# Kernel tuning notes

Measured on AMD Instinct MI355X. Metric: run time of the kernel, lower is better.

The kernel has to match this reference:

```python
import jax, jax.numpy as jnp
import numpy as np

N_NODES, N_EDGES, N_REL, F_DIM, N_HEAD, N_LAYERS = 20000, 100000, 1000, 128, 4, 4
NEG_SLOPE = 0.2  # PyG GATv2Conv default negative_slope


def _gatv2_layer(x, ea_full, src, dst, Wl, bl, Wr, br, We, att, bias):
    # x: [N, F]; ea_full: [Etot, F] edge attrs (incl. self-loop rows)
    N = x.shape[0]
    H, C = att.shape  # heads, out-dim per head
    xl = (x @ Wl + bl).reshape(N, H, C)          # source-side projection
    xr = (x @ Wr + br).reshape(N, H, C)          # target-side projection
    ee = (ea_full @ We).reshape(-1, H, C)        # [Etot, H, C] edge embedding
    # GATv2 scoring: leaky_relu(x_i + x_j + e) . att
    e = jax.nn.leaky_relu(xl[src] + xr[dst] + ee, NEG_SLOPE)
    logits = jnp.einsum('ehc,hc->eh', e, att)    # [Etot, H]
    # segment softmax over edges grouped by destination node
    m = jax.ops.segment_max(logits, dst, num_segments=N)
    p = jnp.exp(logits - m[dst])
    denom = jax.ops.segment_sum(p, dst, num_segments=N)
    alpha = p / denom[dst]                       # [Etot, H]
    out = jax.ops.segment_sum(alpha[:, :, None] * xl[src], dst, num_segments=N)
    return out.mean(axis=1) + bias               # concat=False -> head mean


def setup_inputs() -> dict:
    key = jax.random.key(0)
    ks = jax.random.split(key, 12)
    N, E, R, F, H, L = N_NODES, N_EDGES, N_REL, F_DIM, N_HEAD, N_LAYERS
    HC = H * F
    s = 1.0 / np.sqrt(F)
    return {
        'x': jax.random.normal(ks[0], (N, F), jnp.float32),
        'edge_index': jax.random.randint(ks[1], (2, E), 0, N, dtype=jnp.int32),
        'relations': jax.random.normal(ks[2], (R, F), jnp.float32),
        'relation_index': jax.random.randint(ks[3], (E,), 0, R, dtype=jnp.int32),
        'Wl': jax.random.normal(ks[4], (L, F, HC), jnp.float32) * s,
        'bl': jnp.zeros((L, HC), jnp.float32),
        'Wr': jax.random.normal(ks[5], (L, F, HC), jnp.float32) * s,
        'br': jnp.zeros((L, HC), jnp.float32),
        'We': jax.random.normal(ks[6], (L, F, HC), jnp.float32) * s,
        'att': jax.random.normal(ks[7], (L, H, F), jnp.float32) * s,
        'bias': jnp.zeros((L, F), jnp.float32),
    }


def reference(x, edge_index, relations, relation_index, Wl, bl, Wr, br, We, att, bias):
    N = x.shape[0]
    sl = jnp.arange(N, dtype=edge_index.dtype)
    src = jnp.concatenate([edge_index[0], sl])   # add_self_loops=True
    dst = jnp.concatenate([edge_index[1], sl])
    ea = relations[relation_index]               # [E, F]
    # self-loop edge_attr uses fill_value='mean' (PyG default)
    ea_mean = ea.mean(axis=0)
    ea_full = jnp.concatenate([ea, jnp.broadcast_to(ea_mean, (N, ea.shape[1]))])
    h = x
    for l in range(N_LAYERS):
        h = _gatv2_layer(h, ea_full, src, dst, Wl[l], bl[l], Wr[l], br[l], We[l], att[l], bias[l])
    return (h, relations)
```

## Files before the change

kernel.cpp:

```cpp
#include <hip/hip_runtime.h>
#include <hip/hip_bf16.h>

#define N_NODES   20000
#define N_EDGES   100000
#define N_REL     1000
#define F_DIM     128
#define N_HEAD    4
#define HC        512
#define HC2       256
#define N_LAYERS  4
#define REL_EXT_ROWS 1008
#define NEG_SLOPE 0.2f

typedef __attribute__((ext_vector_type(8))) short short8;
typedef __attribute__((ext_vector_type(4))) float floatx4;

__device__ __forceinline__ float loadIn(const void* p, size_t i, int f32) {
    if (f32) return ((const float*)p)[i];
    union { unsigned int u; float f; } c;
    c.u = ((unsigned int)((const unsigned short*)p)[i]) << 16;
    return c.f;
}

__device__ __forceinline__ unsigned short f2bf(float v) {
    __hip_bfloat16 b = __float2bfloat16(v);
    return *(unsigned short*)&b;
}

__device__ __forceinline__ void unpack2(unsigned int u, float& lo, float& hi) {
    union { unsigned int u; float f; } a, b;
    a.u = u << 16;
    b.u = u & 0xFFFF0000u;
    lo = a.f; hi = b.f;
}

__global__ void detect_kernel(const unsigned short* __restrict__ x, int* __restrict__ flag) {
    int t = threadIdx.x;
    int cnt = 0;
    for (int j = t; j < 256; j += 64) {
        int e = (x[j] >> 7) & 0xFF;
        if (e >= 143) cnt++;
    }
    for (int off = 32; off; off >>= 1) cnt += __shfl_xor(cnt, off);
    if (t == 0) flag[0] = (cnt >= 8) ? 1 : 0;
}


__global__ void hist_kernel(const int* __restrict__ dst, const int* __restrict__ rel,
                            int* __restrict__ deg, int* __restrict__ rcount) {
    int e = blockIdx.x * 256 + threadIdx.x;
    if (e < N_EDGES) {
        atomicAdd(&deg[dst[e]], 1);
        atomicAdd(&rcount[rel[e]], 1);
    }
}

__global__ void ea_mean_kernel(const int* __restrict__ rcount,
                               const void* __restrict__ relations,
                               float* __restrict__ ea_mean, const int* __restrict__ flag) {
    int f32 = flag[0];
    int b = blockIdx.x;
    int t = threadIdx.x;
    int col = t & 127;
    int rhalf = t >> 7;
    float acc = 0.f;
    for (int j = 0; j < 4; ++j) {
        int r = b * 8 + j * 2 + rhalf;
        acc += (float)rcount[r] * loadIn(relations, (size_t)r * F_DIM + col, f32);
    }
    __shared__ float part[256];
    part[t] = acc;
    __syncthreads();
    if (t < 128)
        atomicAdd(&ea_mean[col], (part[t] + part[t + 128]) * (1.f / (float)N_EDGES));
}

__global__ void relext_kernel(const void* __restrict__ relations,
                              const float* __restrict__ ea_mean,
                              unsigned short* __restrict__ rel_ext, const int* __restrict__ flag) {
    int idx = blockIdx.x * 256 + threadIdx.x;
    if (idx >= REL_EXT_ROWS * F_DIM) return;
    int f32 = flag[0];
    int r = idx >> 7;
    int c = idx & 127;
    float v;
    if (r < N_REL)       v = loadIn(relations, idx, f32);
    else if (r == N_REL) v = ea_mean[c];
    else                 v = 0.f;
    rel_ext[idx] = f2bf(v);
}

__global__ void scan_kernel(const int* __restrict__ deg,
                            int* __restrict__ row_start, int* __restrict__ cursor) {
    __shared__ int part[1024];
    int t = threadIdx.x;
    const int CH = (N_NODES + 1023) / 1024;
    int base = t * CH;
    int sum = 0;
    for (int j = 0; j < CH; ++j) {
        int idx = base + j;
        if (idx < N_NODES) sum += deg[idx];
    }
    part[t] = sum;
    __syncthreads();
    for (int off = 1; off < 1024; off <<= 1) {
        int u = (t >= off) ? part[t - off] : 0;
        __syncthreads();
        part[t] += u;
        __syncthreads();
    }
    int run = part[t] - sum;
    for (int j = 0; j < CH; ++j) {
        int idx = base + j;
        if (idx < N_NODES) {
            row_start[idx] = run;
            cursor[idx] = run;
            run += deg[idx];
        }
    }
    if (t == 1023) row_start[N_NODES] = part[1023];
}

__global__ void scatter_kernel(const int* __restrict__ src, const int* __restrict__ dst,
                               const int* __restrict__ rel, int* __restrict__ cursor,
                               int* __restrict__ csr_pack) {
    int e = blockIdx.x * 256 + threadIdx.x;
    if (e < N_EDGES) {
        int d = dst[e];
        int p = atomicAdd(&cursor[d], 1);
        csr_pack[p] = src[e] | (rel[e] << 16);
    }
}

__global__ void tail_kernel(const void* __restrict__ relations, void* __restrict__ out,
                            const int* __restrict__ flag) {
    int i = blockIdx.x * 256 + threadIdx.x;
    if (i >= N_REL * F_DIM) return;
    int f32 = flag[0];
    float v = loadIn(relations, i, f32);
    size_t o = (size_t)N_NODES * F_DIM + i;
    if (f32) ((float*)out)[o] = v;
    else     ((unsigned short*)out)[o] = f2bf(v);
}

__global__ void w_transpose_kernel(const void* __restrict__ Wl, const void* __restrict__ Wr,
                                   const void* __restrict__ We,
                                   unsigned short* __restrict__ Wt, const int* __restrict__ flag) {
    int f32 = flag[0];
    int k0 = blockIdx.x * 64;
    int n0 = blockIdx.y * 64;
    int mat = blockIdx.z;
    const void* src = (mat < 4) ? Wl : (mat < 8 ? Wr : We);
    size_t base = (size_t)(mat & 3) * F_DIM * HC;
    unsigned short* dst = Wt + (size_t)mat * HC * F_DIM;
    __shared__ float T[64][65];
    int t = threadIdx.x;
    int r = t >> 2, cq = t & 3;
    for (int j = 0; j < 16; ++j) {
        int n = cq * 16 + j;
        T[n][r] = loadIn(src, base + (size_t)(k0 + r) * HC + n0 + n, f32);
    }
    __syncthreads();
    for (int j = 0; j < 16; ++j) {
        int k = cq * 16 + j;
        dst[(size_t)(n0 + r) * F_DIM + k0 + k] = f2bf(T[r][k]);
    }
}

__launch_bounds__(256, 4)
__global__ void proj_kernel(const void* __restrict__ A, int a_input, int M,
                            const unsigned short* __restrict__ Wt0,
                            const unsigned short* __restrict__ Wt1,
                            const void* __restrict__ bias0, size_t b0_off,
                            const void* __restrict__ bias1, size_t b1_off,
                            unsigned short* __restrict__ out0,
                            unsigned short* __restrict__ out1,
                            int tpb, const int* __restrict__ flag) {
    __shared__ __align__(16) short As[64][136];
    __shared__ __align__(16) short BtRaw[128 * 72];
    int f32 = flag[0];
    int a_f32 = a_input ? f32 : 0;
    int m0 = blockIdx.x * 64;
    int t = threadIdx.x;

    for (int j = 0; j < 4; ++j) {
        int c = t + j * 256;
        int row = c >> 4;
        int colc = (c & 15) * 8;
        int gm = m0 + row;
        short8 v = (short8){0, 0, 0, 0, 0, 0, 0, 0};
        if (gm < M) {
            size_t idx = (size_t)gm * F_DIM + colc;
            if (a_f32) {
                const float* Af = (const float*)A;
                for (int q = 0; q < 8; ++q) v[q] = (short)f2bf(Af[idx + q]);
            } else {
                v = *(const short8*)((const unsigned short*)A + idx);
            }
        }
        *(short8*)&As[row][colc] = v;
    }

    int wave = t >> 6, lane = t & 63;
    int wm = (wave >> 1) * 32, wn = (wave & 1) * 64;
    int r16 = lane & 15, quad = lane >> 4;

    for (int it = 0; it < tpb; ++it) {
        int nt = blockIdx.y * tpb + it;
        const unsigned short* Wt = (nt < 4) ? Wt0 : Wt1;
        int n0 = (nt & 3) * 128;

        floatx4 acc[2][4];
        for (int mi = 0; mi < 2; ++mi)
            for (int ni = 0; ni < 4; ++ni)
                acc[mi][ni] = (floatx4){0.f, 0.f, 0.f, 0.f};

        for (int half = 0; half < 2; ++half) {
            __syncthreads();
            for (int j = 0; j < 4; ++j) {
                int c = t + j * 256;
                int nl = c >> 3;
                int kc = (c & 7) * 8;
                *(short8*)&BtRaw[nl * 72 + kc] =
                    *(const short8*)(Wt + (size_t)(n0 + nl) * F_DIM + half * 64 + kc);
            }
            __syncthreads();

            for (int kk = 0; kk < 2; ++kk) {
                short8 a[2], b[4];
                for (int mi = 0; mi < 2; ++mi)
                    a[mi] = *(const short8*)&As[wm + mi * 16 + r16][half * 64 + kk * 32 + quad * 8];
                for (int ni = 0; ni < 4; ++ni)
                    b[ni] = *(const short8*)&BtRaw[(wn + ni * 16 + r16) * 72 + kk * 32 + quad * 8];
                for (int mi = 0; mi < 2; ++mi)
                    for (int ni = 0; ni < 4; ++ni)
                        acc[mi][ni] = __builtin_amdgcn_mfma_f32_16x16x32_bf16(a[mi], b[ni], acc[mi][ni], 0, 0, 0);
            }
        }

        const void* bias = (nt < 4) ? bias0 : bias1;
        size_t boff = (nt < 4) ? b0_off : b1_off;
        unsigned short* out = (nt < 4) ? out0 : out1;
        __syncthreads();
        for (int mi = 0; mi < 2; ++mi) {
            for (int ni = 0; ni < 4; ++ni) {
                int col = wn + ni * 16 + r16;
                float bv = bias ? loadIn(bias, boff + n0 + col, f32) : 0.f;
                for (int r = 0; r < 4; ++r) {
                    int rowl = wm + mi * 16 + quad * 4 + r;
                    BtRaw[rowl * 136 + col] = (short)f2bf(acc[mi][ni][r] + bv);
                }
            }
        }
        __syncthreads();
        for (int j = 0; j < 4; ++j) {
            int c = t + j * 256;
            int rowl = c >> 4;
            int colc = (c & 15) * 8;
            int gm = m0 + rowl;
            if (gm < M)
                *(short8*)(out + (size_t)gm * HC + n0 + colc) =
                    *(const short8*)&BtRaw[rowl * 136 + colc];
        }
    }
}

__launch_bounds__(256)
__global__ void edge_kernel(const unsigned int* __restrict__ xl2,
                            const unsigned int* __restrict__ xr2,
                            const unsigned int* __restrict__ re2,
                            const int* __restrict__ row_start,
                            const int* __restrict__ csr_pack,
                            const void* __restrict__ att, size_t att_off,
                            const void* __restrict__ bias, size_t bias_off,
                            void* __restrict__ hout, int final_layer,
                            const int* __restrict__ flag) {
    int f32 = flag[0];
    int i = blockIdx.x;
    int h = threadIdx.x >> 6;
    int lane = threadIdx.x & 63;
    int pidx = h * 64 + lane;

    float xr0, xr1; unpack2(xr2[(size_t)i * HC2 + pidx], xr0, xr1);
    float a0 = loadIn(att, att_off + h * F_DIM + 2 * lane, f32);
    float a1 = loadIn(att, att_off + h * F_DIM + 2 * lane + 1, f32);
    float er0, er1; unpack2(re2[(size_t)N_REL * HC2 + pidx], er0, er1);

    float xs0, xs1; unpack2(xl2[(size_t)i * HC2 + pidx], xs0, xs1);
    float t0 = xs0 + xr0 + er0;
    float t1 = xs1 + xr1 + er1;
    t0 = (t0 > 0.f) ? t0 : NEG_SLOPE * t0;
    t1 = (t1 > 0.f) ? t1 : NEG_SLOPE * t1;
    float m = t0 * a0 + t1 * a1;
    for (int off = 32; off; off >>= 1) m += __shfl_xor(m, off);
    float s = 1.f, acc0 = xs0, acc1 = xs1;

    int e0 = row_start[i], e1 = row_start[i + 1];
    if (e0 < 0) e0 = 0;
    if (e1 > N_EDGES) e1 = N_EDGES;
    if (e1 < e0) e1 = e0;

    unsigned int xlv = 0, rev = 0;
    if (e0 < e1) {
        int pk = csr_pack[e0];
        int src = pk & 0xFFFF;  if (src >= N_NODES) src = 0;
        int rr  = (pk >> 16) & 0x3FF; if (rr > N_REL) rr = N_REL;
        xlv = xl2[(size_t)src * HC2 + pidx];
        rev = re2[(size_t)rr * HC2 + pidx];
    }
    for (int e = e0; e < e1; ++e) {
        unsigned int xlvn = 0, revn = 0;
        if (e + 1 < e1) {
            int pkn = csr_pack[e + 1];
            int sn = pkn & 0xFFFF;  if (sn >= N_NODES) sn = 0;
            int rn = (pkn >> 16) & 0x3FF; if (rn > N_REL) rn = N_REL;
            xlvn = xl2[(size_t)sn * HC2 + pidx];
            revn = re2[(size_t)rn * HC2 + pidx];
        }
        float xl0, xl1; unpack2(xlv, xl0, xl1);
        float ee0, ee1; unpack2(rev, ee0, ee1);
        float u0 = xl0 + xr0 + ee0;
        float u1 = xl1 + xr1 + ee1;
        u0 = (u0 > 0.f) ? u0 : NEG_SLOPE * u0;
        u1 = (u1 > 0.f) ? u1 : NEG_SLOPE * u1;
        float part = u0 * a0 + u1 * a1;
        for (int off = 32; off; off >>= 1) part += __shfl_xor(part, off);
        float mn = fmaxf(m, part);
        float sc = __expf(m - mn);
        float p  = __expf(part - mn);
        s = s * sc + p;
        acc0 = acc0 * sc + p * xl0;
        acc1 = acc1 * sc + p * xl1;
        m = mn;
        xlv = xlvn; rev = revn;
    }

    float inv = 1.f / s;
    __shared__ float lsum[N_HEAD][F_DIM];
    lsum[h][2 * lane]     = acc0 * inv;
    lsum[h][2 * lane + 1] = acc1 * inv;
    __syncthreads();
    if (threadIdx.x < F_DIM) {
        int c = threadIdx.x;
        float v = (lsum[0][c] + lsum[1][c] + lsum[2][c] + lsum[3][c]) * 0.25f
                + loadIn(bias, bias_off + c, f32);
        size_t o = (size_t)i * F_DIM + c;
        if (final_layer && f32) ((float*)hout)[o] = v;
        else                    ((unsigned short*)hout)[o] = f2bf(v);
    }
}


extern "C" void kernel_launch(void* const* d_in, const int* in_sizes, int n_in,
                              void* d_out, int out_size, void* d_ws, size_t ws_size,
                              hipStream_t stream) {
    const void* x          = d_in[0];
    const int*  edge_index = (const int*)d_in[1];
    const void* relations  = d_in[2];
    const int*  rel_index  = (const int*)d_in[3];
    const void* Wl         = d_in[4];
    const void* bl         = d_in[5];
    const void* Wr         = d_in[6];
    const void* br         = d_in[7];
    const void* We         = d_in[8];
    const void* att        = d_in[9];
    const void* bias       = d_in[10];

    char* ws = (char*)d_ws;
    size_t off = 0;
    auto alloc = [&](size_t bytes) -> void* {
        void* p = ws + off;
        off = (off + bytes + 255) & ~(size_t)255;
        return p;
    };
    int*            flag     = (int*)alloc(4);
    int*            deg      = (int*)alloc(N_NODES * 4);
    int*            row_start= (int*)alloc((N_NODES + 1) * 4);
    int*            cursor   = (int*)alloc(N_NODES * 4);
    int*            rcount   = (int*)alloc(N_REL * 4);
    float*          ea_mean  = (float*)alloc(F_DIM * 4);
    int*            csr_pack = (int*)alloc(N_EDGES * 4);
    unsigned short* rel_ext  = (unsigned short*)alloc((size_t)REL_EXT_ROWS * F_DIM * 2);
    unsigned short* Wt       = (unsigned short*)alloc((size_t)12 * HC * F_DIM * 2);
    unsigned short* re       = (unsigned short*)alloc((size_t)REL_EXT_ROWS * HC * 2);
    unsigned short* hbuf     = (unsigned short*)alloc((size_t)N_NODES * F_DIM * 2);
    unsigned short* xl       = (unsigned short*)alloc((size_t)N_NODES * HC * 2);
    unsigned short* xr       = (unsigned short*)alloc((size_t)N_NODES * HC * 2);

    const int* esrc = edge_index;
    const int* edst = edge_index + N_EDGES;

    detect_kernel<<<1, 64, 0, stream>>>((const unsigned short*)x, flag);
    hipMemsetAsync(rcount, 0, N_REL * 4, stream);
    hipMemsetAsync(deg, 0, N_NODES * 4, stream);
    hipMemsetAsync(ea_mean, 0, F_DIM * 4, stream);
    hist_kernel<<<(N_EDGES + 255) / 256, 256, 0, stream>>>(edst, rel_index, deg, rcount);
    ea_mean_kernel<<<N_REL / 8, 256, 0, stream>>>(rcount, relations, ea_mean, flag);
    relext_kernel<<<(REL_EXT_ROWS * F_DIM + 255) / 256, 256, 0, stream>>>(relations, ea_mean, rel_ext, flag);
    scan_kernel<<<1, 1024, 0, stream>>>(deg, row_start, cursor);
    scatter_kernel<<<(N_EDGES + 255) / 256, 256, 0, stream>>>(esrc, edst, rel_index, cursor, csr_pack);
    w_transpose_kernel<<<dim3(2, 8, 12), 256, 0, stream>>>(Wl, Wr, We, Wt, flag);
    tail_kernel<<<(N_REL * F_DIM + 255) / 256, 256, 0, stream>>>(relations, d_out, flag);

    const void* hin = x;
    int a_input = 1;
    for (int l = 0; l < N_LAYERS; ++l) {
        const unsigned short* Wlt = Wt + (size_t)l * HC * F_DIM;
        const unsigned short* Wrt = Wt + (size_t)(4 + l) * HC * F_DIM;
        const unsigned short* Wet = Wt + (size_t)(8 + l) * HC * F_DIM;
        proj_kernel<<<dim3((N_NODES + 63) / 64, 4), 256, 0, stream>>>(
            hin, a_input, N_NODES, Wlt, Wrt,
            bl, (size_t)l * HC, br, (size_t)l * HC,
            xl, xr, 2, flag);
        proj_kernel<<<dim3((REL_EXT_ROWS + 63) / 64, 4), 256, 0, stream>>>(
            rel_ext, 0, REL_EXT_ROWS, Wet, nullptr,
            nullptr, 0, nullptr, 0,
            re, nullptr, 1, flag);
        int final_layer = (l == N_LAYERS - 1);
        void* hout = final_layer ? d_out : (void*)hbuf;
        edge_kernel<<<N_NODES, 256, 0, stream>>>((const unsigned int*)xl, (const unsigned int*)xr,
                                                 (const unsigned int*)re, row_start, csr_pack,
                                                 att, (size_t)l * N_HEAD * F_DIM,
                                                 bias, (size_t)l * F_DIM,
                                                 hout, final_layer, flag);
        hin = hbuf;
        a_input = 0;
    }
}
```

Measured before the change: 494.7 us.

## Parallelize edge softmax across wavefronts with chunked two-pass shared-memory logits

The edge kernel now spreads a node's incoming edges across the four wavefronts. Each wavefront handles a whole edge row using 16-byte vector loads, so all four heads are covered in one load, instead of one wavefront per head walking every edge serially. Logits are staged in shared memory in chunks of up to 256 edges, and a block-wide max/sum pass produces the softmax weights. A second pass re-gathers the source features to accumulate the weighted sums, and the partial sums are then reduced across wavefronts. This removes the serial, latency-bound online-softmax loop but adds extra gathers of xl, more block synchronisations and more shared-memory traffic.

Result: slower. 701.3 us (+41.8%).

```diff
diff --git a/kernel.cpp b/kernel.cpp
--- a/kernel.cpp
+++ b/kernel.cpp
@@ -11,6 +11,7 @@
 #define N_LAYERS  4
 #define REL_EXT_ROWS 1008
 #define NEG_SLOPE 0.2f
+#define MAXE      256
 
 typedef __attribute__((ext_vector_type(8))) short short8;
 typedef __attribute__((ext_vector_type(4))) float floatx4;
@@ -275,75 +276,130 @@
                             const void* __restrict__ bias, size_t bias_off,
                             void* __restrict__ hout, int final_layer,
                             const int* __restrict__ flag) {
+    __shared__ float l_log[N_HEAD][MAXE];
+    __shared__ float l_acc[N_HEAD][HC / N_HEAD * N_HEAD];
+    __shared__ float s_run[N_HEAD], m_run[N_HEAD], chunk_sc[N_HEAD];
+
     int f32 = flag[0];
     int i = blockIdx.x;
-    int h = threadIdx.x >> 6;
-    int lane = threadIdx.x & 63;
-    int pidx = h * 64 + lane;
-
-    float xr0, xr1; unpack2(xr2[(size_t)i * HC2 + pidx], xr0, xr1);
-    float a0 = loadIn(att, att_off + h * F_DIM + 2 * lane, f32);
-    float a1 = loadIn(att, att_off + h * F_DIM + 2 * lane + 1, f32);
-    float er0, er1; unpack2(re2[(size_t)N_REL * HC2 + pidx], er0, er1);
-
-    float xs0, xs1; unpack2(xl2[(size_t)i * HC2 + pidx], xs0, xs1);
-    float t0 = xs0 + xr0 + er0;
-    float t1 = xs1 + xr1 + er1;
-    t0 = (t0 > 0.f) ? t0 : NEG_SLOPE * t0;
-    t1 = (t1 > 0.f) ? t1 : NEG_SLOPE * t1;
-    float m = t0 * a0 + t1 * a1;
-    for (int off = 32; off; off >>= 1) m += __shfl_xor(m, off);
-    float s = 1.f, acc0 = xs0, acc1 = xs1;
+    int t = threadIdx.x;
+    int w = t >> 6, lane = t & 63;
+    int hl = lane >> 4;
+
+    const uint4* xl4 = (const uint4*)xl2;
+    const uint4* re4 = (const uint4*)re2;
+    const uint4* xr4 = (const uint4*)xr2;
+
+    float xrv[8], attv[8];
+    {
+        uint4 u = xr4[(size_t)i * 64 + lane];
+        unpack2(u.x, xrv[0], xrv[1]); unpack2(u.y, xrv[2], xrv[3]);
+        unpack2(u.z, xrv[4], xrv[5]); unpack2(u.w, xrv[6], xrv[7]);
+        for (int q = 0; q < 8; ++q)
+            attv[q] = loadIn(att, att_off + lane * 8 + q, f32);
+    }
+
+    if (t < N_HEAD) { s_run[t] = 0.f; m_run[t] = -3.0e38f; }
 
     int e0 = row_start[i], e1 = row_start[i + 1];
     if (e0 < 0) e0 = 0;
     if (e1 > N_EDGES) e1 = N_EDGES;
     if (e1 < e0) e1 = e0;
-
-    unsigned int xlv = 0, rev = 0;
-    if (e0 < e1) {
-        int pk = csr_pack[e0];
-        int src = pk & 0xFFFF;  if (src >= N_NODES) src = 0;
-        int rr  = (pk >> 16) & 0x3FF; if (rr > N_REL) rr = N_REL;
-        xlv = xl2[(size_t)src * HC2 + pidx];
-        rev = re2[(size_t)rr * HC2 + pidx];
-    }
-    for (int e = e0; e < e1; ++e) {
-        unsigned int xlvn = 0, revn = 0;
-        if (e + 1 < e1) {
-            int pkn = csr_pack[e + 1];
-            int sn = pkn & 0xFFFF;  if (sn >= N_NODES) sn = 0;
-            int rn = (pkn >> 16) & 0x3FF; if (rn > N_REL) rn = N_REL;
-            xlvn = xl2[(size_t)sn * HC2 + pidx];
-            revn = re2[(size_t)rn * HC2 + pidx];
-        }
-        float xl0, xl1; unpack2(xlv, xl0, xl1);
-        float ee0, ee1; unpack2(rev, ee0, ee1);
-        float u0 = xl0 + xr0 + ee0;
-        float u1 = xl1 + xr1 + ee1;
-        u0 = (u0 > 0.f) ? u0 : NEG_SLOPE * u0;
-        u1 = (u1 > 0.f) ? u1 : NEG_SLOPE * u1;
-        float part = u0 * a0 + u1 * a1;
-        for (int off = 32; off; off >>= 1) part += __shfl_xor(part, off);
-        float mn = fmaxf(m, part);
-        float sc = __expf(m - mn);
-        float p  = __expf(part - mn);
-        s = s * sc + p;
-        acc0 = acc0 * sc + p * xl0;
-        acc1 = acc1 * sc + p * xl1;
-        m = mn;
-        xlv = xlvn; rev = revn;
-    }
-
-    float inv = 1.f / s;
-    __shared__ float lsum[N_HEAD][F_DIM];
-    lsum[h][2 * lane]     = acc0 * inv;
-    lsum[h][2 * lane + 1] = acc1 * inv;
+    int total = (e1 - e0) + 1;
+    int nchunks = (total + MAXE - 1) / MAXE;
+
+    float acc[8];
+    for (int q = 0; q < 8; ++q) acc[q] = 0.f;
+
+    for (int ck = 0; ck < nchunks; ++ck) {
+        int start = ck * MAXE;
+        int cnt = total - start; if (cnt > MAXE) cnt = MAXE;
+        __syncthreads();
+
+        for (int slot = w; slot < cnt; slot += 4) {
+            int gs = start + slot;
+            int src, rr;
+            if (gs == 0) { src = i; rr = N_REL; }
+            else {
+                int pk = csr_pack[e0 + gs - 1];
+                src = pk & 0xFFFF;            if (src >= N_NODES) src = 0;
+                rr  = (pk >> 16) & 0x3FF;     if (rr > N_REL) rr = N_REL;
+            }
+            uint4 xu = xl4[(size_t)src * 64 + lane];
+            uint4 ru = re4[(size_t)rr * 64 + lane];
+            float xv[8], rv[8];
+            unpack2(xu.x, xv[0], xv[1]); unpack2(xu.y, xv[2], xv[3]);
+            unpack2(xu.z, xv[4], xv[5]); unpack2(xu.w, xv[6], xv[7]);
+            unpack2(ru.x, rv[0], rv[1]); unpack2(ru.y, rv[2], rv[3]);
+            unpack2(ru.z, rv[4], rv[5]); unpack2(ru.w, rv[6], rv[7]);
+            float part = 0.f;
+            for (int q = 0; q < 8; ++q) {
+                float u = xv[q] + xrv[q] + rv[q];
+                u = (u > 0.f) ? u : NEG_SLOPE * u;
+                part += u * attv[q];
+            }
+            for (int off = 8; off; off >>= 1) part += __shfl_xor(part, off);
+            if ((lane & 15) == 0) l_log[hl][slot] = part;
+        }
+        __syncthreads();
+
+        {
+            float cmax = -3.0e38f;
+            for (int sl = lane; sl < cnt; sl += 64) cmax = fmaxf(cmax, l_log[w][sl]);
+            for (int off = 32; off; off >>= 1) cmax = fmaxf(cmax, __shfl_xor(cmax, off));
+            float csum = 0.f;
+            for (int sl = lane; sl < cnt; sl += 64) {
+                float p = __expf(l_log[w][sl] - cmax);
+                l_log[w][sl] = p;
+                csum += p;
+            }
+            for (int off = 32; off; off >>= 1) csum += __shfl_xor(csum, off);
+            float mo = m_run[w];
+            float mn = fmaxf(mo, cmax);
+            float sc = __expf(mo - mn);
+            float fc = __expf(cmax - mn);
+            if (lane == 0) {
+                s_run[w] = s_run[w] * sc + fc * csum;
+                m_run[w] = mn;
+                chunk_sc[w] = sc;
+            }
+            for (int sl = lane; sl < cnt; sl += 64) l_log[w][sl] *= fc;
+        }
+        __syncthreads();
+
+        {
+            float scw = chunk_sc[hl];
+            for (int q = 0; q < 8; ++q) acc[q] *= scw;
+        }
+        for (int slot = w; slot < cnt; slot += 4) {
+            int gs = start + slot;
+            int src;
+            if (gs == 0) src = i;
+            else {
+                int pk = csr_pack[e0 + gs - 1];
+                src = pk & 0xFFFF; if (src >= N_NODES) src = 0;
+            }
+            uint4 xu = xl4[(size_t)src * 64 + lane];
+            float p = l_log[hl][slot];
+            float xv[8];
+            unpack2(xu.x, xv[0], xv[1]); unpack2(xu.y, xv[2], xv[3]);
+            unpack2(xu.z, xv[4], xv[5]); unpack2(xu.w, xv[6], xv[7]);
+            for (int q = 0; q < 8; ++q) acc[q] += p * xv[q];
+        }
+    }
+
     __syncthreads();
-    if (threadIdx.x < F_DIM) {
-        int c = threadIdx.x;
-        float v = (lsum[0][c] + lsum[1][c] + lsum[2][c] + lsum[3][c]) * 0.25f
-                + loadIn(bias, bias_off + c, f32);
+    for (int q = 0; q < 8; ++q) l_acc[w][lane * 8 + q] = acc[q];
+    __syncthreads();
+    if (t < F_DIM) {
+        int c = t;
+        float v = 0.f;
+        for (int h = 0; h < N_HEAD; ++h) {
+            float a = l_acc[0][h * F_DIM + c] + l_acc[1][h * F_DIM + c]
+                    + l_acc[2][h * F_DIM + c] + l_acc[3][h * F_DIM + c];
+            v += a / s_run[h];
+        }
+        v = v * 0.25f + loadIn(bias, bias_off + c, f32);
         size_t o = (size_t)i * F_DIM + c;
         if (final_layer && f32) ((float*)hout)[o] = v;
         else                    ((unsigned short*)hout)[o] = f2bf(v);
```

## Split fused edge kernel into edge-parallel scoring and node-parallel aggregation

Applied to the files above, without the earlier changes.

Replaces the per-node online-softmax edge kernel with two kernels. The first computes attention logits for every edge, including self-loops, with one wavefront per edge using 16-byte vector loads, and writes them to a logits buffer. The second does a two-pass softmax per destination node over the stored logits, then a weighted sum of gathered source features. This aims to parallelise scoring across edges instead of serialising it per node, at the cost of an extra launch per layer, a logits round trip through memory, a csr_dst array, and a second gather of xl in aggregation.

Result: slower. 923.1 us (+86.6%).

```diff
diff --git a/kernel.cpp b/kernel.cpp
--- a/kernel.cpp
+++ b/kernel.cpp
@@ -123,12 +123,13 @@
 
 __global__ void scatter_kernel(const int* __restrict__ src, const int* __restrict__ dst,
                                const int* __restrict__ rel, int* __restrict__ cursor,
-                               int* __restrict__ csr_pack) {
+                               int* __restrict__ csr_pack, int* __restrict__ csr_dst) {
     int e = blockIdx.x * 256 + threadIdx.x;
     if (e < N_EDGES) {
         int d = dst[e];
         int p = atomicAdd(&cursor[d], 1);
         csr_pack[p] = src[e] | (rel[e] << 16);
+        csr_dst[p] = d;
     }
 }
 
@@ -266,82 +267,103 @@
 }
 
 __launch_bounds__(256)
-__global__ void edge_kernel(const unsigned int* __restrict__ xl2,
-                            const unsigned int* __restrict__ xr2,
-                            const unsigned int* __restrict__ re2,
-                            const int* __restrict__ row_start,
-                            const int* __restrict__ csr_pack,
-                            const void* __restrict__ att, size_t att_off,
-                            const void* __restrict__ bias, size_t bias_off,
-                            void* __restrict__ hout, int final_layer,
-                            const int* __restrict__ flag) {
+__global__ void score_kernel(const uint4* __restrict__ xl4, const uint4* __restrict__ xr4,
+                             const uint4* __restrict__ re4,
+                             const int* __restrict__ csr_pack, const int* __restrict__ csr_dst,
+                             const void* __restrict__ att, size_t att_off,
+                             float* __restrict__ logits, const int* __restrict__ flag) {
+    int f32 = flag[0];
+    int w = threadIdx.x >> 6, lane = threadIdx.x & 63;
+    int v = blockIdx.x * 4 + w;
+    if (v >= N_EDGES + N_NODES) return;
+    int src, dst, rr;
+    if (v < N_EDGES) {
+        int pk = csr_pack[v];
+        src = pk & 0xFFFF;        if (src >= N_NODES) src = 0;
+        rr  = (pk >> 16) & 0x3FF; if (rr > N_REL) rr = N_REL;
+        dst = csr_dst[v];         if (dst < 0 || dst >= N_NODES) dst = 0;
+    } else {
+        src = dst = v - N_EDGES;
+        rr = N_REL;
+    }
+    uint4 xu = xl4[(size_t)src * 64 + lane];
+    uint4 yu = xr4[(size_t)dst * 64 + lane];
+    uint4 ru = re4[(size_t)rr * 64 + lane];
+    float xv[8], yv[8], rv[8];
+    unpack2(xu.x, xv[0], xv[1]); unpack2(xu.y, xv[2], xv[3]);
+    unpack2(xu.z, xv[4], xv[5]); unpack2(xu.w, xv[6], xv[7]);
+    unpack2(yu.x, yv[0], yv[1]); unpack2(yu.y, yv[2], yv[3]);
+    unpack2(yu.z, yv[4], yv[5]); unpack2(yu.w, yv[6], yv[7]);
+    unpack2(ru.x, rv[0], rv[1]); unpack2(ru.y, rv[2], rv[3]);
+    unpack2(ru.z, rv[4], rv[5]); unpack2(ru.w, rv[6], rv[7]);
+    float part = 0.f;
+    for (int q = 0; q < 8; ++q) {
+        float u = xv[q] + yv[q] + rv[q];
+        u = (u > 0.f) ? u : NEG_SLOPE * u;
+        part += u * loadIn(att, att_off + lane * 8 + q, f32);
+    }
+    for (int off = 8; off; off >>= 1) part += __shfl_xor(part, off);
+    if ((lane & 15) == 0) logits[(size_t)v * 4 + (lane >> 4)] = part;
+}
+
+__launch_bounds__(256)
+__global__ void agg_kernel(const unsigned int* __restrict__ xl2,
+                           const int* __restrict__ row_start,
+                           const int* __restrict__ csr_pack,
+                           const float* __restrict__ logits,
+                           const void* __restrict__ bias, size_t bias_off,
+                           void* __restrict__ hout, int final_layer,
+                           const int* __restrict__ flag) {
+    __shared__ float lsum[N_HEAD][F_DIM];
     int f32 = flag[0];
     int i = blockIdx.x;
-    int h = threadIdx.x >> 6;
-    int lane = threadIdx.x & 63;
-    int pidx = h * 64 + lane;
-
-    float xr0, xr1; unpack2(xr2[(size_t)i * HC2 + pidx], xr0, xr1);
-    float a0 = loadIn(att, att_off + h * F_DIM + 2 * lane, f32);
-    float a1 = loadIn(att, att_off + h * F_DIM + 2 * lane + 1, f32);
-    float er0, er1; unpack2(re2[(size_t)N_REL * HC2 + pidx], er0, er1);
-
-    float xs0, xs1; unpack2(xl2[(size_t)i * HC2 + pidx], xs0, xs1);
-    float t0 = xs0 + xr0 + er0;
-    float t1 = xs1 + xr1 + er1;
-    t0 = (t0 > 0.f) ? t0 : NEG_SLOPE * t0;
-    t1 = (t1 > 0.f) ? t1 : NEG_SLOPE * t1;
-    float m = t0 * a0 + t1 * a1;
-    for (int off = 32; off; off >>= 1) m += __shfl_xor(m, off);
-    float s = 1.f, acc0 = xs0, acc1 = xs1;
+    int t = threadIdx.x, w = t >> 6, lane = t & 63;
+    int pidx = w * 64 + lane;
 
     int e0 = row_start[i], e1 = row_start[i + 1];
     if (e0 < 0) e0 = 0;
     if (e1 > N_EDGES) e1 = N_EDGES;
     if (e1 < e0) e1 = e0;
-
-    unsigned int xlv = 0, rev = 0;
-    if (e0 < e1) {
-        int pk = csr_pack[e0];
-        int src = pk & 0xFFFF;  if (src >= N_NODES) src = 0;
-        int rr  = (pk >> 16) & 0x3FF; if (rr > N_REL) rr = N_REL;
-        xlv = xl2[(size_t)src * HC2 + pidx];
-        rev = re2[(size_t)rr * HC2 + pidx];
-    }
-    for (int e = e0; e < e1; ++e) {
-        unsigned int xlvn = 0, revn = 0;
-        if (e + 1 < e1) {
-            int pkn = csr_pack[e + 1];
-            int sn = pkn & 0xFFFF;  if (sn >= N_NODES) sn = 0;
-            int rn = (pkn >> 16) & 0x3FF; if (rn > N_REL) rn = N_REL;
-            xlvn = xl2[(size_t)sn * HC2 + pidx];
-            revn = re2[(size_t)rn * HC2 + pidx];
-        }
-        float xl0, xl1; unpack2(xlv, xl0, xl1);
-        float ee0, ee1; unpack2(rev, ee0, ee1);
-        float u0 = xl0 + xr0 + ee0;
-        float u1 = xl1 + xr1 + ee1;
-        u0 = (u0 > 0.f) ? u0 : NEG_SLOPE * u0;
-        u1 = (u1 > 0.f) ? u1 : NEG_SLOPE * u1;
-        float part = u0 * a0 + u1 * a1;
-        for (int off = 32; off; off >>= 1) part += __shfl_xor(part, off);
-        float mn = fmaxf(m, part);
-        float sc = __expf(m - mn);
-        float p  = __expf(part - mn);
-        s = s * sc + p;
-        acc0 = acc0 * sc + p * xl0;
-        acc1 = acc1 * sc + p * xl1;
-        m = mn;
-        xlv = xlvn; rev = revn;
-    }
-
-    float inv = 1.f / s;
-    __shared__ float lsum[N_HEAD][F_DIM];
-    lsum[h][2 * lane]     = acc0 * inv;
-    lsum[h][2 * lane + 1] = acc1 * inv;
+    int cnt = (e1 - e0) + 1;
+
+    float mx = -3.0e38f;
+    for (int sl = lane; sl < cnt; sl += 64) {
+        float lg = (sl == 0) ? logits[((size_t)N_EDGES + i) * 4 + w]
+                             : logits[(size_t)(e0 + sl - 1) * 4 + w];
+        mx = fmaxf(mx, lg);
+    }
+    for (int off = 32; off; off >>= 1) mx = fmaxf(mx, __shfl_xor(mx, off));
+    float sm = 0.f;
+    for (int sl = lane; sl < cnt; sl += 64) {
+        float lg = (sl == 0) ? logits[((size_t)N_EDGES + i) * 4 + w]
+                             : logits[(size_t)(e0 + sl - 1) * 4 + w];
+        sm += __expf(lg - mx);
+    }
+    for (int off = 32; off; off >>= 1) sm += __shfl_xor(sm, off);
+
+    float acc0 = 0.f, acc1 = 0.f;
+    float lgc = logits[((size_t)N_EDGES + i) * 4 + w];
+    unsigned int uc = xl2[(size_t)i * HC2 + pidx];
+    for (int slot = 0; slot < cnt; ++slot) {
+        float lgn = 0.f; unsigned int un = 0;
+        if (slot + 1 < cnt) {
+            int pk = csr_pack[e0 + slot];
+            int sn = pk & 0xFFFF; if (sn >= N_NODES) sn = 0;
+            lgn = logits[(size_t)(e0 + slot) * 4 + w];
+            un = xl2[(size_t)sn * HC2 + pidx];
+        }
+        float p = __expf(lgc - mx);
+        float v0, v1; unpack2(uc, v0, v1);
+        acc0 += p * v0;
+        acc1 += p * v1;
+        lgc = lgn; uc = un;
+    }
+    float inv = 1.f / sm;
+    lsum[w][2 * lane]     = acc0 * inv;
+    lsum[w][2 * lane + 1] = acc1 * inv;
     __syncthreads();
-    if (threadIdx.x < F_DIM) {
-        int c = threadIdx.x;
+    if (t < F_DIM) {
+        int c = t;
         float v = (lsum[0][c] + lsum[1][c] + lsum[2][c] + lsum[3][c]) * 0.25f
                 + loadIn(bias, bias_off + c, f32);
         size_t o = (size_t)i * F_DIM + c;
@@ -380,6 +402,8 @@
     int*            rcount   = (int*)alloc(N_REL * 4);
     float*          ea_mean  = (float*)alloc(F_DIM * 4);
     int*            csr_pack = (int*)alloc(N_EDGES * 4);
+    int*            csr_dst  = (int*)alloc(N_EDGES * 4);
+    float*          logits   = (float*)alloc((size_t)(N_EDGES + N_NODES) * 4 * 4);
     unsigned short* rel_ext  = (unsigned short*)alloc((size_t)REL_EXT_ROWS * F_DIM * 2);
     unsigned short* Wt       = (unsigned short*)alloc((size_t)12 * HC * F_DIM * 2);
     unsigned short* re       = (unsigned short*)alloc((size_t)REL_EXT_ROWS * HC * 2);
@@ -398,10 +422,12 @@
     ea_mean_kernel<<<N_REL / 8, 256, 0, stream>>>(rcount, relations, ea_mean, flag);
     relext_kernel<<<(REL_EXT_ROWS * F_DIM + 255) / 256, 256, 0, stream>>>(relations, ea_mean, rel_ext, flag);
     scan_kernel<<<1, 1024, 0, stream>>>(deg, row_start, cursor);
-    scatter_kernel<<<(N_EDGES + 255) / 256, 256, 0, stream>>>(esrc, edst, rel_index, cursor, csr_pack);
+    scatter_kernel<<<(N_EDGES + 255) / 256, 256, 0, stream>>>(esrc, edst, rel_index, cursor,
+                                                              csr_pack, csr_dst);
     w_transpose_kernel<<<dim3(2, 8, 12), 256, 0, stream>>>(Wl, Wr, We, Wt, flag);
     tail_kernel<<<(N_REL * F_DIM + 255) / 256, 256, 0, stream>>>(relations, d_out, flag);
 
+    const int score_blocks = (N_EDGES + N_NODES + 3) / 4;
     const void* hin = x;
     int a_input = 1;
     for (int l = 0; l < N_LAYERS; ++l) {
@@ -416,13 +442,14 @@
             rel_ext, 0, REL_EXT_ROWS, Wet, nullptr,
             nullptr, 0, nullptr, 0,
             re, nullptr, 1, flag);
+        score_kernel<<<score_blocks, 256, 0, stream>>>(
+            (const uint4*)xl, (const uint4*)xr, (const uint4*)re,
+            csr_pack, csr_dst, att, (size_t)l * N_HEAD * F_DIM, logits, flag);
         int final_layer = (l == N_LAYERS - 1);
         void* hout = final_layer ? d_out : (void*)hbuf;
-        edge_kernel<<<N_NODES, 256, 0, stream>>>((const unsigned int*)xl, (const unsigned int*)xr,
-                                                 (const unsigned int*)re, row_start, csr_pack,
-                                                 att, (size_t)l * N_HEAD * F_DIM,
-                                                 bias, (size_t)l * F_DIM,
-                                                 hout, final_layer, flag);
+        agg_kernel<<<N_NODES, 256, 0, stream>>>(
+            (const unsigned int*)xl, row_start, csr_pack, logits,
+            bias, (size_t)l * F_DIM, hout, final_layer, flag);
         hin = hbuf;
         a_input = 0;
     }
```

## Merge node and relation projections into one launch; drop online-softmax max tracking

Applied to the files above, without the earlier changes.

The node projection (xl/xr) and the relation-embedding projection are combined into a single proj_kernel launch. The block index decides which operand set each block works on, which saves one launch per layer and lets the small relation GEMM fill the tail of the node GEMM. The edge kernel's online softmax, which rescaled by a running max, becomes a plain sum of exp over logits clamped to [-60, 60]. This removes two exps and the rescale multiplies per edge, but relies on the clamp to keep values in range, which could change results if logits ever exceed that range.

Result: faster. 465.9 us (-5.8%).

```diff
diff --git a/kernel.cpp b/kernel.cpp
--- a/kernel.cpp
+++ b/kernel.cpp
@@ -11,6 +11,8 @@
 #define N_LAYERS  4
 #define REL_EXT_ROWS 1008
 #define NEG_SLOPE 0.2f
+#define NODE_MB   ((N_NODES + 63) / 64)
+#define REL_MB    ((REL_EXT_ROWS + 63) / 64)
 
 typedef __attribute__((ext_vector_type(8))) short short8;
 typedef __attribute__((ext_vector_type(4))) float floatx4;
@@ -168,19 +170,26 @@
 }
 
 __launch_bounds__(256, 4)
-__global__ void proj_kernel(const void* __restrict__ A, int a_input, int M,
-                            const unsigned short* __restrict__ Wt0,
-                            const unsigned short* __restrict__ Wt1,
-                            const void* __restrict__ bias0, size_t b0_off,
-                            const void* __restrict__ bias1, size_t b1_off,
-                            unsigned short* __restrict__ out0,
-                            unsigned short* __restrict__ out1,
-                            int tpb, const int* __restrict__ flag) {
+__global__ void proj_kernel(const void* __restrict__ A_node, int a_input,
+                            const unsigned short* __restrict__ rel_ext,
+                            const unsigned short* __restrict__ Wlt,
+                            const unsigned short* __restrict__ Wrt,
+                            const unsigned short* __restrict__ Wet,
+                            const void* __restrict__ bl, const void* __restrict__ br,
+                            size_t boff,
+                            unsigned short* __restrict__ xl,
+                            unsigned short* __restrict__ xr,
+                            unsigned short* __restrict__ re,
+                            const int* __restrict__ flag) {
     __shared__ __align__(16) short As[64][136];
     __shared__ __align__(16) short BtRaw[128 * 72];
     int f32 = flag[0];
-    int a_f32 = a_input ? f32 : 0;
-    int m0 = blockIdx.x * 64;
+    int isNode = (blockIdx.x < NODE_MB);
+    int m0 = (isNode ? blockIdx.x : (blockIdx.x - NODE_MB)) * 64;
+    int M = isNode ? N_NODES : REL_EXT_ROWS;
+    int tpb = isNode ? 2 : 1;
+    int a_f32 = (isNode && a_input) ? f32 : 0;
+    const void* A = isNode ? A_node : (const void*)rel_ext;
     int t = threadIdx.x;
 
     for (int j = 0; j < 4; ++j) {
@@ -206,8 +215,8 @@
     int r16 = lane & 15, quad = lane >> 4;
 
     for (int it = 0; it < tpb; ++it) {
-        int nt = blockIdx.y * tpb + it;
-        const unsigned short* Wt = (nt < 4) ? Wt0 : Wt1;
+        int nt = isNode ? (blockIdx.y * 2 + it) : blockIdx.y;
+        const unsigned short* Wt = isNode ? ((nt < 4) ? Wlt : Wrt) : Wet;
         int n0 = (nt & 3) * 128;
 
         floatx4 acc[2][4];
@@ -238,9 +247,8 @@
             }
         }
 
-        const void* bias = (nt < 4) ? bias0 : bias1;
-        size_t boff = (nt < 4) ? b0_off : b1_off;
-        unsigned short* out = (nt < 4) ? out0 : out1;
+        const void* bias = isNode ? ((nt < 4) ? bl : br) : nullptr;
+        unsigned short* out = isNode ? ((nt < 4) ? xl : xr) : re;
         __syncthreads();
         for (int mi = 0; mi < 2; ++mi) {
             for (int ni = 0; ni < 4; ++ni) {
@@ -289,11 +297,13 @@
     float xs0, xs1; unpack2(xl2[(size_t)i * HC2 + pidx], xs0, xs1);
     float t0 = xs0 + xr0 + er0;
     float t1 = xs1 + xr1 + er1;
-    t0 = (t0 > 0.f) ? t0 : NEG_SLOPE * t0;
-    t1 = (t1 > 0.f) ? t1 : NEG_SLOPE * t1;
-    float m = t0 * a0 + t1 * a1;
-    for (int off = 32; off; off >>= 1) m += __shfl_xor(m, off);
-    float s = 1.f, acc0 = xs0, acc1 = xs1;
+    t0 = fmaxf(t0, NEG_SLOPE * t0);
+    t1 = fmaxf(t1, NEG_SLOPE * t1);
+    float part = t0 * a0 + t1 * a1;
+    for (int off = 32; off; off >>= 1) part += __shfl_xor(part, off);
+    part = fminf(fmaxf(part, -60.f), 60.f);
+    float p = __expf(part);
+    float s = p, acc0 = p * xs0, acc1 = p * xs1;
 
     int e0 = row_start[i], e1 = row_start[i + 1];
     if (e0 < 0) e0 = 0;
@@ -321,17 +331,15 @@
         float ee0, ee1; unpack2(rev, ee0, ee1);
         float u0 = xl0 + xr0 + ee0;
         float u1 = xl1 + xr1 + ee1;
-        u0 = (u0 > 0.f) ? u0 : NEG_SLOPE * u0;
-        u1 = (u1 > 0.f) ? u1 : NEG_SLOPE * u1;
-        float part = u0 * a0 + u1 * a1;
-        for (int off = 32; off; off >>= 1) part += __shfl_xor(part, off);
-        float mn = fmaxf(m, part);
-        float sc = __expf(m - mn);
-        float p  = __expf(part - mn);
-        s = s * sc + p;
-        acc0 = acc0 * sc + p * xl0;
-        acc1 = acc1 * sc + p * xl1;
-        m = mn;
+        u0 = fmaxf(u0, NEG_SLOPE * u0);
+        u1 = fmaxf(u1, NEG_SLOPE * u1);
+        float pe = u0 * a0 + u1 * a1;
+        for (int off = 32; off; off >>= 1) pe += __shfl_xor(pe, off);
+        pe = fminf(fmaxf(pe, -60.f), 60.f);
+        float pp = __expf(pe);
+        s += pp;
+        acc0 += pp * xl0;
+        acc1 += pp * xl1;
         xlv = xlvn; rev = revn;
     }
 
@@ -408,21 +416,18 @@
         const unsigned short* Wlt = Wt + (size_t)l * HC * F_DIM;
         const unsigned short* Wrt = Wt + (size_t)(4 + l) * HC * F_DIM;
         const unsigned short* Wet = Wt + (size_t)(8 + l) * HC * F_DIM;
-        proj_kernel<<<dim3((N_NODES + 63) / 64, 4), 256, 0, stream>>>(
-            hin, a_input, N_NODES, Wlt, Wrt,
-            bl, (size_t)l * HC, br, (size_t)l * HC,
-            xl, xr, 2, flag);
-        proj_kernel<<<dim3((REL_EXT_ROWS + 63) / 64, 4), 256, 0, stream>>>(
-            rel_ext, 0, REL_EXT_ROWS, Wet, nullptr,
-            nullptr, 0, nullptr, 0,
-            re, nullptr, 1, flag);
+        proj_kernel<<<dim3(NODE_MB + REL_MB, 4), 256, 0, stream>>>(
+            hin, a_input, rel_ext, Wlt, Wrt, Wet,
+            bl, br, (size_t)l * HC,
+            xl, xr, re, flag);
         int final_layer = (l == N_LAYERS - 1);
         void* hout = final_layer ? d_out : (void*)hbuf;
-        edge_kernel<<<N_NODES, 256, 0, stream>>>((const unsigned int*)xl, (const unsigned int*)xr,
-                                                 (const unsigned int*)re, row_start, csr_pack,
-                                                 att, (size_t)l * N_HEAD * F_DIM,
-                                                 bias, (size_t)l * F_DIM,
-                                                 hout, final_layer, flag);
+        edge_kernel<<<N_NODES, 256, 0, stream>>>(
+            (const unsigned int*)xl, (const unsigned int*)xr, (const unsigned int*)re,
+            row_start, csr_pack,
+            att, (size_t)l * N_HEAD * F_DIM,
+            bias, (size_t)l * F_DIM,
+            hout, final_layer, flag);
         hin = hbuf;
         a_input = 0;
     }
```
